# Kernel tuning notes

Measured on AMD Instinct MI355X. Metric: run time of the kernel, lower is better.

The kernel has to match this reference:

```python
import jax, jax.numpy as jnp
import numpy as np

B, L, D, E, K = 8, 384, 1024, 4, 2
H = 4 * D  # expert MLP hidden


def setup_inputs() -> dict:
    key = jax.random.key(0)
    ks = jax.random.split(key, 10)
    def w(k, shape, fan_in):
        return jax.random.normal(k, shape, jnp.float32) / np.sqrt(fan_in).astype(np.float32)
    return {
        "context_c": jax.random.normal(ks[0], (B, L, D), jnp.float32),
        "time_cond": jax.random.normal(ks[1], (B, D), jnp.float32),
        "gate_W": w(ks[2], (E, 3 * D), 3 * D),
        "gate_b": jnp.zeros((E,), jnp.float32),
        "tmod_W": w(ks[3], (2 * E, D), D),
        "tmod_b": jnp.zeros((2 * E,), jnp.float32),
        "eW1": w(ks[4], (E, D, H), D),
        "eb1": jnp.zeros((E, H), jnp.float32),
        "eW2": w(ks[5], (E, H, D), H),
        "eb2": jnp.zeros((E, D), jnp.float32),
        "sW1": w(ks[6], (D, H), D),
        "sb1": jnp.zeros((H,), jnp.float32),
        "sW2": w(ks[7], (H, D), H),
        "sb2": jnp.zeros((D,), jnp.float32),
    }


def reference(context_c, time_cond, gate_W, gate_b, tmod_W, tmod_b,
              eW1, eb1, eW2, eb2, sW1, sb1, sW2, sb2):
    Lh = Lw = L // 3
    Lp = L - Lh - Lw
    head = context_c[:, :Lh]            # (B, Lh, D)
    wrist = context_c[:, Lh:Lh + Lw]    # (B, Lw, D)
    prop = context_c[:, Lh + Lw:]       # (B, Lp, D)

    # per-sample modality-combo aggregates for the gate
    full_agg = context_c.mean(axis=1)
    hp_agg = (head.sum(axis=1) + prop.sum(axis=1)) / (Lh + Lp)
    wp_agg = (wrist.sum(axis=1) + prop.sum(axis=1)) / (Lw + Lp)
    gate_in = jnp.concatenate([full_agg, hp_agg, wp_agg], axis=-1)  # (B, 3D)

    logits = gate_in @ gate_W.T + gate_b                            # (B, E)
    mod = jax.nn.silu(time_cond) @ tmod_W.T + tmod_b                # (B, 2E)
    scale, shift = mod[:, :E], mod[:, E:]
    logits = logits * (1.0 + scale) + shift

    scores = jax.nn.softmax(logits, axis=-1)
    tw, ti = jax.lax.top_k(scores, K)                               # (B, K)
    tw = tw / (tw.sum(axis=-1, keepdims=True) + 1e-8)
    # per-sample combined weight for each expert: (B, E)
    w_be = (jax.nn.one_hot(ti, E, dtype=tw.dtype) * tw[..., None]).sum(axis=1)

    # modality mask per expert (E, L): expert 1 skips wrist, expert 2 skips head
    mask_np = np.ones((E, L), np.float32)
    mask_np[1, Lh:Lh + Lw] = 0.0
    mask_np[2, :Lh] = 0.0
    mask = jnp.asarray(mask_np)

    # run all experts on all tokens (token-wise MLP), combine with per-sample
    # routing weights and per-expert modality masks — identical math to the
    # original per-sample sliced dispatch.
    h = jax.nn.gelu(jnp.einsum('bld,edh->belh', context_c, eW1)
                    + eb1[None, :, None, :], approximate=True)      # (B,E,L,H)
    y = jnp.einsum('belh,ehd->beld', h, eW2) + eb2[None, :, None, :]
    out = jnp.einsum('be,el,beld->bld', w_be, mask, y)

    # shared expert (always-on)
    shared = jax.nn.gelu(context_c @ sW1 + sb1, approximate=True) @ sW2 + sb2
    return out + shared
```

## Files before the change

kernel.cpp:

```cpp
#include <hip/hip_runtime.h>
#include <cstdint>
#include <cstddef>


#define DEV __device__ __forceinline__

typedef __attribute__((ext_vector_type(8))) __bf16 bf16x8;
typedef __attribute__((ext_vector_type(4))) __bf16 bf16x4;
typedef __attribute__((ext_vector_type(4))) float f32x4;

static constexpr int Bb = 8, Ll = 384, Dd = 1024, Ee = 4, Hh = 4096;

DEV void load_lds16(const void* g, void* l) {
  __builtin_amdgcn_global_load_lds(
      (const __attribute__((address_space(1))) void*)g,
      (__attribute__((address_space(3))) void*)l, 16, 0, 0);
}

DEV float gelu_tanh(float x) {
  float u = 0.7978845608028654f * (x + 0.044715f * x * x * x);
  float t = 1.0f - 2.0f / (1.0f + __expf(2.0f * u));
  return 0.5f * x * (1.0f + t);
}

DEV float wave_red(float v) {
#pragma unroll
  for (int o = 32; o > 0; o >>= 1) v += __shfl_down(v, o, 64);
  return v;
}


__global__ void cvt_x_kernel(const float* __restrict__ src, __bf16* __restrict__ dst, int n4) {
  int i = blockIdx.x * blockDim.x + threadIdx.x;
  if (i >= n4) return;
  float4 v = ((const float4*)src)[i];
  bf16x4 o;
  o.x = (__bf16)v.x; o.y = (__bf16)v.y; o.z = (__bf16)v.z; o.w = (__bf16)v.w;
  ((bf16x4*)dst)[i] = o;
}

__global__ void transpose_cvt_kernel(const float* __restrict__ src, __bf16* __restrict__ dst,
                                     int nr, int nc) {
  __shared__ float t[32][33];
  size_t base = (size_t)blockIdx.z * nr * nc;
  src += base; dst += base;
  int x = threadIdx.x & 31, y = threadIdx.x >> 5;
  int c0 = blockIdx.x * 32, r0 = blockIdx.y * 32;
#pragma unroll
  for (int r = 0; r < 4; ++r) {
    int rr = y + r * 8;
    t[rr][x] = src[(size_t)(r0 + rr) * nc + c0 + x];
  }
  __syncthreads();
#pragma unroll
  for (int r = 0; r < 4; ++r) {
    int rr = y + r * 8;
    dst[(size_t)(c0 + rr) * nr + r0 + x] = (__bf16)t[x][rr];
  }
}


__global__ void agg_kernel(const float* __restrict__ ctx, float* __restrict__ part) {
  int c = blockIdx.x, b = blockIdx.y, t = threadIdx.x;
  int d0 = t * 4;
  float4 sum = {0.f, 0.f, 0.f, 0.f};
  const float* p = ctx + ((size_t)(b * Ll + c * 64)) * Dd + d0;
  for (int l = 0; l < 64; ++l) {
    float4 v = *(const float4*)(p + (size_t)l * Dd);
    sum.x += v.x; sum.y += v.y; sum.z += v.z; sum.w += v.w;
  }
  *(float4*)(part + ((size_t)(b * 6 + c)) * Dd + d0) = sum;
}

__global__ void gate_kernel(const float* __restrict__ part, const float* __restrict__ tc,
                            const float* __restrict__ gW, const float* __restrict__ gb,
                            const float* __restrict__ tW, const float* __restrict__ tb,
                            int* __restrict__ slotE, float* __restrict__ slotW) {
  __shared__ float gi[3 * Dd];
  __shared__ float st[Dd];
  __shared__ float red[12];
  int b = blockIdx.x, t = threadIdx.x;
  const float* pb = part + (size_t)b * 6 * Dd;
#pragma unroll
  for (int k = 0; k < 4; ++k) {
    int d = t * 4 + k;
    float p0 = pb[d], p1 = pb[Dd + d], p2 = pb[2 * Dd + d];
    float p3 = pb[3 * Dd + d], p4 = pb[4 * Dd + d], p5 = pb[5 * Dd + d];
    gi[d]          = (p0 + p1 + p2 + p3 + p4 + p5) * (1.0f / 384.0f);
    gi[Dd + d]     = (p0 + p1 + p4 + p5) * (1.0f / 256.0f);
    gi[2 * Dd + d] = (p2 + p3 + p4 + p5) * (1.0f / 256.0f);
    float tv = tc[b * Dd + d];
    st[d] = tv / (1.0f + __expf(-tv));
  }
  __syncthreads();
  int wid = t >> 6, lane = t & 63;
  float aL = 0.f;
  for (int i = lane; i < 3 * Dd; i += 64) aL += gi[i] * gW[wid * 3 * Dd + i];
  aL = wave_red(aL);
  float aA = 0.f, aB = 0.f;
  for (int i = lane; i < Dd; i += 64) {
    float s = st[i];
    aA += s * tW[wid * Dd + i];
    aB += s * tW[(wid + 4) * Dd + i];
  }
  aA = wave_red(aA); aB = wave_red(aB);
  if (lane == 0) { red[wid] = aL; red[4 + wid] = aA; red[8 + wid] = aB; }
  __syncthreads();
  if (t == 0) {
    float lg[4];
#pragma unroll
    for (int e = 0; e < 4; ++e) {
      float logit = red[e] + gb[e];
      float scale = red[4 + e] + tb[e];
      float shift = red[8 + e] + tb[4 + e];
      lg[e] = logit * (1.0f + scale) + shift;
    }
    float m = fmaxf(fmaxf(lg[0], lg[1]), fmaxf(lg[2], lg[3]));
    float p[4], sum = 0.f;
#pragma unroll
    for (int e = 0; e < 4; ++e) { p[e] = __expf(lg[e] - m); sum += p[e]; }
#pragma unroll
    for (int e = 0; e < 4; ++e) p[e] /= sum;
    int i0 = 0;
    for (int e = 1; e < 4; ++e) if (p[e] > p[i0]) i0 = e;
    int i1 = -1;
    for (int e = 0; e < 4; ++e) if (e != i0 && (i1 < 0 || p[e] > p[i1])) i1 = e;
    float sw = p[i0] + p[i1] + 1e-8f;
    slotE[b * 4 + 0] = i0; slotE[b * 4 + 1] = i1;
    slotW[b * 4 + 0] = p[i0] / sw; slotW[b * 4 + 1] = p[i1] / sw;
  }
}


__global__ __launch_bounds__(256) void gemm1_kernel(
    const __bf16* __restrict__ Xbf, const __bf16* __restrict__ W1T,
    const __bf16* __restrict__ S1T, const float* __restrict__ eb1,
    const float* __restrict__ sb1, const int* __restrict__ slotE,
    const float* __restrict__ slotW, __bf16* __restrict__ Hbuf, int bbase) {
  constexpr int K = Dd;
  int bid = blockIdx.x, nwg = gridDim.x;
  int lid = (bid & 7) * (nwg >> 3) + (bid >> 3);
  int nt = lid & 31;
  int r = lid >> 5;
  int mt = r % 3; r /= 3;
  int s = r % 3;
  int bl = r / 3;
  int b = bbase + bl;
  int e = (s == 2) ? Ee : slotE[b * 4 + s];
  if ((e == 1 && mt == 1) || (e == 2 && mt == 0)) return;
  float wgt = (s == 2) ? 1.0f : slotW[b * 4 + s];

  const __bf16* Ab = Xbf + ((size_t)(b * Ll + mt * 128)) * K;
  const __bf16* Bbp = (e < Ee ? W1T + (size_t)e * Hh * K : S1T) + (size_t)(nt * 128) * K;
  const float* b1p = (e < Ee ? eb1 + e * Hh : sb1);

  __shared__ __align__(16) char smem[65536];

  int tid = threadIdx.x, wid = tid >> 6, lane = tid & 63;
  int q = lane >> 4, l16 = lane & 15;
  int wm = wid >> 1, wn = wid & 1;

  const __bf16* gp[8];
  uint32_t lo[8];
#pragma unroll
  for (int u = 0; u < 8; ++u) {
    int c = wid * 8 + u;
    int isB = c >> 4;
    int blk = (c & 15) >> 1;
    int ks = c & 1;
    const __bf16* base = isB ? Bbp : Ab;
    gp[u] = base + (size_t)(blk * 16 + l16) * K + ks * 32 + q * 8;
    lo[u] = (uint32_t)(isB * 16384 + (blk * 2 + ks) * 1024);
  }

  f32x4 acc[4][4];
  f32x4 zero = {0.f, 0.f, 0.f, 0.f};
#pragma unroll
  for (int i = 0; i < 4; ++i)
#pragma unroll
    for (int j = 0; j < 4; ++j) acc[i][j] = zero;

#pragma unroll
  for (int u = 0; u < 8; ++u) load_lds16(gp[u], smem + lo[u]);

  constexpr int NK = K / 64;
  for (int kt = 0; kt < NK; ++kt) {
    int ph = kt & 1;
    __syncthreads();
    if (kt + 1 < NK) {
#pragma unroll
      for (int u = 0; u < 8; ++u) {
        gp[u] += 64;
        load_lds16(gp[u], smem + lo[u] + (ph ^ 1) * 32768);
      }
    }
    const char* sm = (const char*)smem + ph * 32768;
#pragma unroll
    for (int ks = 0; ks < 2; ++ks) {
      bf16x8 a[4], bb[4];
#pragma unroll
      for (int i = 0; i < 4; ++i)
        a[i] = *(const bf16x8*)(sm + (((wm * 4 + i) * 2 + ks) * 64 + lane) * 16);
#pragma unroll
      for (int j = 0; j < 4; ++j)
        bb[j] = *(const bf16x8*)(sm + 16384 + (((wn * 4 + j) * 2 + ks) * 64 + lane) * 16);
#pragma unroll
      for (int i = 0; i < 4; ++i)
#pragma unroll
        for (int j = 0; j < 4; ++j)
          acc[i][j] = __builtin_amdgcn_mfma_f32_16x16x32_bf16(a[i], bb[j], acc[i][j], 0, 0, 0);
    }
  }

  float bias[4];
#pragma unroll
  for (int j = 0; j < 4; ++j) bias[j] = b1p[nt * 128 + wn * 64 + j * 16 + l16];

  __syncthreads();
  __bf16* tile = (__bf16*)smem;
#pragma unroll
  for (int i = 0; i < 4; ++i)
#pragma unroll
    for (int j = 0; j < 4; ++j)
#pragma unroll
      for (int r2 = 0; r2 < 4; ++r2) {
        float x = acc[i][j][r2] + bias[j];
        int row = wm * 64 + i * 16 + q * 4 + r2;
        int col = wn * 64 + j * 16 + l16;
        tile[row * 136 + col] = (__bf16)(wgt * gelu_tanh(x));
      }
  __syncthreads();
  __bf16* Hrow = Hbuf + ((size_t)(bl * 3 + s) * Ll + mt * 128) * Hh + nt * 128;
#pragma unroll
  for (int t2 = 0; t2 < 8; ++t2) {
    int gidx = t2 * 256 + tid;
    int row = gidx >> 4, cg = gidx & 15;
    bf16x8 v = *(const bf16x8*)(tile + row * 136 + cg * 8);
    *(bf16x8*)(Hrow + (size_t)row * Hh + cg * 8) = v;
  }
}


template <int KC>
__global__ __launch_bounds__(256) void gemm2_kernel(
    const __bf16* __restrict__ Hbuf, const __bf16* __restrict__ W2T,
    const __bf16* __restrict__ S2T, const float* __restrict__ eb2,
    const float* __restrict__ sb2, const int* __restrict__ slotE,
    const float* __restrict__ slotW, float* __restrict__ out,
    __bf16* __restrict__ pbuf, int bbase, int bc) {
  constexpr int K = Hh;
  constexpr int NKC = Hh / KC;
  int bid = blockIdx.x, nwg = gridDim.x;
  int lid = (bid & 7) * (nwg >> 3) + (bid >> 3);
  int nt = lid & 7;
  int r = lid >> 3;
  int mt = r % 3; r /= 3;
  int kc = r % NKC;
  int bl = r / NKC;
  int b = bbase + bl;

  __shared__ __align__(16) char smem[65536];

  int tid = threadIdx.x, wid = tid >> 6, lane = tid & 63;
  int q = lane >> 4, l16 = lane & 15;
  int wm = wid >> 1, wn = wid & 1;

  f32x4 acc[4][4];
  f32x4 zero = {0.f, 0.f, 0.f, 0.f};
#pragma unroll
  for (int i = 0; i < 4; ++i)
#pragma unroll
    for (int j = 0; j < 4; ++j) acc[i][j] = zero;
  float biasacc[4] = {0.f, 0.f, 0.f, 0.f};

  for (int s = 0; s < 3; ++s) {
    int e = (s == 2) ? Ee : slotE[b * 4 + s];
    if ((e == 1 && mt == 1) || (e == 2 && mt == 0)) continue;
    float wgt = (s == 2) ? 1.0f : slotW[b * 4 + s];

    const __bf16* Ab = Hbuf + ((size_t)(bl * 3 + s) * Ll + mt * 128) * K + (size_t)kc * KC;
    const __bf16* Bbp = (e < Ee ? W2T + (size_t)e * Dd * K : S2T) + (size_t)(nt * 128) * K + (size_t)kc * KC;

    const __bf16* gp[8];
    uint32_t lo[8];
#pragma unroll
    for (int u = 0; u < 8; ++u) {
      int c = wid * 8 + u;
      int isB = c >> 4;
      int blk = (c & 15) >> 1;
      int ks = c & 1;
      const __bf16* base = isB ? Bbp : Ab;
      gp[u] = base + (size_t)(blk * 16 + l16) * K + ks * 32 + q * 8;
      lo[u] = (uint32_t)(isB * 16384 + (blk * 2 + ks) * 1024);
    }

#pragma unroll
    for (int u = 0; u < 8; ++u) load_lds16(gp[u], smem + lo[u]);

    constexpr int NK = KC / 64;
    for (int kt = 0; kt < NK; ++kt) {
      int ph = kt & 1;
      __syncthreads();
      if (kt + 1 < NK) {
#pragma unroll
        for (int u = 0; u < 8; ++u) {
          gp[u] += 64;
          load_lds16(gp[u], smem + lo[u] + (ph ^ 1) * 32768);
        }
      }
      const char* sm = (const char*)smem + ph * 32768;
#pragma unroll
      for (int ks = 0; ks < 2; ++ks) {
        bf16x8 a[4], bb[4];
#pragma unroll
        for (int i = 0; i < 4; ++i)
          a[i] = *(const bf16x8*)(sm + (((wm * 4 + i) * 2 + ks) * 64 + lane) * 16);
#pragma unroll
        for (int j = 0; j < 4; ++j)
          bb[j] = *(const bf16x8*)(sm + 16384 + (((wn * 4 + j) * 2 + ks) * 64 + lane) * 16);
#pragma unroll
        for (int i = 0; i < 4; ++i)
#pragma unroll
          for (int j = 0; j < 4; ++j)
            acc[i][j] = __builtin_amdgcn_mfma_f32_16x16x32_bf16(a[i], bb[j], acc[i][j], 0, 0, 0);
      }
    }

    if (kc == 0) {
      const float* b2p = (e < Ee ? eb2 + e * Dd : sb2);
#pragma unroll
      for (int j = 0; j < 4; ++j)
        biasacc[j] += wgt * b2p[nt * 128 + wn * 64 + j * 16 + l16];
    }
  }

  if (pbuf) {
    __syncthreads();
    __bf16* tile = (__bf16*)smem;
#pragma unroll
    for (int i = 0; i < 4; ++i)
#pragma unroll
      for (int j = 0; j < 4; ++j)
#pragma unroll
        for (int r2 = 0; r2 < 4; ++r2) {
          int row = wm * 64 + i * 16 + q * 4 + r2;
          int col = wn * 64 + j * 16 + l16;
          tile[row * 136 + col] = (__bf16)(acc[i][j][r2] + biasacc[j]);
        }
    __syncthreads();
    __bf16* Prow = pbuf + (((size_t)(kc * bc + bl) * Ll + mt * 128)) * Dd + nt * 128;
#pragma unroll
    for (int t2 = 0; t2 < 8; ++t2) {
      int gidx = t2 * 256 + tid;
      int row = gidx >> 4, cg = gidx & 15;
      bf16x8 v = *(const bf16x8*)(tile + row * 136 + cg * 8);
      *(bf16x8*)(Prow + (size_t)row * Dd + cg * 8) = v;
    }
  } else {
    float* orow = out + ((size_t)(b * Ll + mt * 128)) * Dd + nt * 128;
#pragma unroll
    for (int i = 0; i < 4; ++i)
#pragma unroll
      for (int j = 0; j < 4; ++j)
#pragma unroll
        for (int r2 = 0; r2 < 4; ++r2) {
          int row = wm * 64 + i * 16 + q * 4 + r2;
          int col = wn * 64 + j * 16 + l16;
          atomicAdd(orow + (size_t)row * Dd + col, acc[i][j][r2] + biasacc[j]);
        }
  }
}

__global__ void reduce_kernel(const __bf16* __restrict__ pbuf, float* __restrict__ out,
                              int n8, size_t stride, int nkc) {
  int i = blockIdx.x * blockDim.x + threadIdx.x;
  if (i >= n8) return;
  size_t base = (size_t)i * 8;
  float sum[8];
#pragma unroll
  for (int k = 0; k < 8; ++k) sum[k] = 0.f;
  for (int kc = 0; kc < nkc; ++kc) {
    bf16x8 v = *(const bf16x8*)(pbuf + kc * stride + base);
#pragma unroll
    for (int k = 0; k < 8; ++k) sum[k] += (float)v[k];
  }
  float4 o0 = {sum[0], sum[1], sum[2], sum[3]};
  float4 o1 = {sum[4], sum[5], sum[6], sum[7]};
  *(float4*)(out + base) = o0;
  *(float4*)(out + base + 4) = o1;
}


extern "C" void kernel_launch(void* const* d_in, const int* in_sizes, int n_in,
                              void* d_out, int out_size, void* d_ws, size_t ws_size,
                              hipStream_t stream) {
  (void)in_sizes; (void)n_in;
  const float* ctx = (const float*)d_in[0];
  const float* tc  = (const float*)d_in[1];
  const float* gW  = (const float*)d_in[2];
  const float* gb  = (const float*)d_in[3];
  const float* tW  = (const float*)d_in[4];
  const float* tb  = (const float*)d_in[5];
  const float* eW1 = (const float*)d_in[6];
  const float* eb1 = (const float*)d_in[7];
  const float* eW2 = (const float*)d_in[8];
  const float* eb2 = (const float*)d_in[9];
  const float* sW1 = (const float*)d_in[10];
  const float* sb1 = (const float*)d_in[11];
  const float* sW2 = (const float*)d_in[12];
  const float* sb2 = (const float*)d_in[13];
  float* out = (float*)d_out;

  char* ws = (char*)d_ws;
  size_t off = 0;
  auto alloc = [&](size_t sz) { size_t o = off; off += (sz + 255) & ~(size_t)255; return o; };
  size_t oW1T = alloc((size_t)Ee * Hh * Dd * 2);
  size_t oW2T = alloc((size_t)Ee * Dd * Hh * 2);
  size_t oS1T = alloc((size_t)Hh * Dd * 2);
  size_t oS2T = alloc((size_t)Dd * Hh * 2);
  size_t oX   = alloc((size_t)Bb * Ll * Dd * 2);
  size_t oP   = alloc((size_t)Bb * 6 * Dd * 4);
  size_t oSE  = alloc(Bb * 4 * sizeof(int));
  size_t oSW  = alloc(Bb * 4 * sizeof(float));
  size_t fixed = off;

  auto hbufB = [&](int bc) { return (size_t)bc * 3 * Ll * Hh * 2; };
  auto pbufB = [&](int bc, int nkc) { return (size_t)nkc * bc * Ll * Dd * 2; };
  int bc = 1; bool use_pbuf = false; int nkc = 4;
  if (fixed + hbufB(8) + pbufB(8, 8) + 512 <= ws_size)      { bc = 8; use_pbuf = true; nkc = 8; }
  else if (fixed + hbufB(8) + pbufB(8, 4) + 512 <= ws_size) { bc = 8; use_pbuf = true; nkc = 4; }
  else if (fixed + hbufB(4) + pbufB(4, 4) + 512 <= ws_size) { bc = 4; use_pbuf = true; nkc = 4; }
  else if (fixed + hbufB(4) + 512 <= ws_size)               { bc = 4; use_pbuf = false; nkc = 4; }
  else if (fixed + hbufB(2) + 512 <= ws_size)               { bc = 2; use_pbuf = false; nkc = 4; }
  else                                                      { bc = 1; use_pbuf = false; nkc = 4; }
  int nchunk = Bb / bc;
  size_t oH = alloc(hbufB(bc));
  size_t oPB = use_pbuf ? alloc(pbufB(bc, nkc)) : 0;

  __bf16* W1T = (__bf16*)(ws + oW1T);
  __bf16* W2T = (__bf16*)(ws + oW2T);
  __bf16* S1T = (__bf16*)(ws + oS1T);
  __bf16* S2T = (__bf16*)(ws + oS2T);
  __bf16* Xbf = (__bf16*)(ws + oX);
  float*  part = (float*)(ws + oP);
  int*    slotE = (int*)(ws + oSE);
  float*  slotW = (float*)(ws + oSW);
  __bf16* Hbuf = (__bf16*)(ws + oH);
  __bf16* Pbuf = use_pbuf ? (__bf16*)(ws + oPB) : nullptr;

  if (!use_pbuf)
    hipMemsetAsync(d_out, 0, (size_t)out_size * sizeof(float), stream);

  cvt_x_kernel<<<(Bb * Ll * Dd / 4 + 255) / 256, 256, 0, stream>>>(ctx, Xbf, Bb * Ll * Dd / 4);
  transpose_cvt_kernel<<<dim3(Hh / 32, Dd / 32, Ee), 256, 0, stream>>>(eW1, W1T, Dd, Hh);
  transpose_cvt_kernel<<<dim3(Dd / 32, Hh / 32, Ee), 256, 0, stream>>>(eW2, W2T, Hh, Dd);
  transpose_cvt_kernel<<<dim3(Hh / 32, Dd / 32, 1), 256, 0, stream>>>(sW1, S1T, Dd, Hh);
  transpose_cvt_kernel<<<dim3(Dd / 32, Hh / 32, 1), 256, 0, stream>>>(sW2, S2T, Hh, Dd);
  agg_kernel<<<dim3(6, Bb), 256, 0, stream>>>(ctx, part);
  gate_kernel<<<Bb, 256, 0, stream>>>(part, tc, gW, gb, tW, tb, slotE, slotW);

  for (int c = 0; c < nchunk; ++c) {
    gemm1_kernel<<<dim3(288 * bc), 256, 0, stream>>>(
        Xbf, W1T, S1T, eb1, sb1, slotE, slotW, Hbuf, c * bc);
    int g2 = 8 * 3 * nkc * bc;
    if (nkc == 8)
      gemm2_kernel<512><<<dim3(g2), 256, 0, stream>>>(
          Hbuf, W2T, S2T, eb2, sb2, slotE, slotW, out, Pbuf, c * bc, bc);
    else
      gemm2_kernel<1024><<<dim3(g2), 256, 0, stream>>>(
          Hbuf, W2T, S2T, eb2, sb2, slotE, slotW, out, Pbuf, c * bc, bc);
    if (use_pbuf) {
      int n8 = bc * Ll * Dd / 8;
      reduce_kernel<<<(n8 + 255) / 256, 256, 0, stream>>>(
          Pbuf, out + (size_t)c * bc * Ll * Dd, n8, (size_t)bc * Ll * Dd, nkc);
    }
  }
}
```

Baseline: 563.2 us.

## Drop LDS double buffering in expert GEMMs to raise occupancy

Both GEMM kernels switch from a double-buffered LDS pipeline (64 KB, prefetching the next K tile during compute) to a single 32 KB buffer (34816 bytes allocated) with load, sync, compute each step. Launch bounds now request 4 workgroups per CU. The aim is to hide global-load latency by running more resident waves instead of explicit prefetch. The cost is an extra barrier per K step and no intra-block overlap of loads with MFMA work.

Result: faster. 549.1 us (-2.5%).

```diff
diff --git a/kernel.cpp b/kernel.cpp
--- a/kernel.cpp
+++ b/kernel.cpp
@@ -132,7 +132,7 @@
 }
 
 
-__global__ __launch_bounds__(256) void gemm1_kernel(
+__global__ __launch_bounds__(256, 4) void gemm1_kernel(
     const __bf16* __restrict__ Xbf, const __bf16* __restrict__ W1T,
     const __bf16* __restrict__ S1T, const float* __restrict__ eb1,
     const float* __restrict__ sb1, const int* __restrict__ slotE,
@@ -154,7 +154,7 @@
   const __bf16* Bbp = (e < Ee ? W1T + (size_t)e * Hh * K : S1T) + (size_t)(nt * 128) * K;
   const float* b1p = (e < Ee ? eb1 + e * Hh : sb1);
 
-  __shared__ __align__(16) char smem[65536];
+  __shared__ __align__(16) char smem[34816];
 
   int tid = threadIdx.x, wid = tid >> 6, lane = tid & 63;
   int q = lane >> 4, l16 = lane & 15;
@@ -180,36 +180,28 @@
 #pragma unroll
     for (int j = 0; j < 4; ++j) acc[i][j] = zero;
 
-#pragma unroll
-  for (int u = 0; u < 8; ++u) load_lds16(gp[u], smem + lo[u]);
-
-  constexpr int NK = K / 64;
-  for (int kt = 0; kt < NK; ++kt) {
-    int ph = kt & 1;
+  for (int kt = 0; kt < K / 64; ++kt) {
     __syncthreads();
-    if (kt + 1 < NK) {
-#pragma unroll
-      for (int u = 0; u < 8; ++u) {
-        gp[u] += 64;
-        load_lds16(gp[u], smem + lo[u] + (ph ^ 1) * 32768);
-      }
-    }
-    const char* sm = (const char*)smem + ph * 32768;
+#pragma unroll
+    for (int u = 0; u < 8; ++u) load_lds16(gp[u], smem + lo[u]);
+    __syncthreads();
 #pragma unroll
     for (int ks = 0; ks < 2; ++ks) {
       bf16x8 a[4], bb[4];
 #pragma unroll
       for (int i = 0; i < 4; ++i)
-        a[i] = *(const bf16x8*)(sm + (((wm * 4 + i) * 2 + ks) * 64 + lane) * 16);
+        a[i] = *(const bf16x8*)(smem + (((wm * 4 + i) * 2 + ks) * 64 + lane) * 16);
 #pragma unroll
       for (int j = 0; j < 4; ++j)
-        bb[j] = *(const bf16x8*)(sm + 16384 + (((wn * 4 + j) * 2 + ks) * 64 + lane) * 16);
+        bb[j] = *(const bf16x8*)(smem + 16384 + (((wn * 4 + j) * 2 + ks) * 64 + lane) * 16);
 #pragma unroll
       for (int i = 0; i < 4; ++i)
 #pragma unroll
         for (int j = 0; j < 4; ++j)
           acc[i][j] = __builtin_amdgcn_mfma_f32_16x16x32_bf16(a[i], bb[j], acc[i][j], 0, 0, 0);
     }
+#pragma unroll
+    for (int u = 0; u < 8; ++u) gp[u] += 64;
   }
 
   float bias[4];
@@ -242,7 +234,7 @@
 
 
 template <int KC>
-__global__ __launch_bounds__(256) void gemm2_kernel(
+__global__ __launch_bounds__(256, 4) void gemm2_kernel(
     const __bf16* __restrict__ Hbuf, const __bf16* __restrict__ W2T,
     const __bf16* __restrict__ S2T, const float* __restrict__ eb2,
     const float* __restrict__ sb2, const int* __restrict__ slotE,
@@ -259,7 +251,7 @@
   int bl = r / NKC;
   int b = bbase + bl;
 
-  __shared__ __align__(16) char smem[65536];
+  __shared__ __align__(16) char smem[34816];
 
   int tid = threadIdx.x, wid = tid >> 6, lane = tid & 63;
   int q = lane >> 4, l16 = lane & 15;
@@ -294,36 +286,28 @@
       lo[u] = (uint32_t)(isB * 16384 + (blk * 2 + ks) * 1024);
     }
 
-#pragma unroll
-    for (int u = 0; u < 8; ++u) load_lds16(gp[u], smem + lo[u]);
-
-    constexpr int NK = KC / 64;
-    for (int kt = 0; kt < NK; ++kt) {
-      int ph = kt & 1;
+    for (int kt = 0; kt < KC / 64; ++kt) {
       __syncthreads();
-      if (kt + 1 < NK) {
-#pragma unroll
-        for (int u = 0; u < 8; ++u) {
-          gp[u] += 64;
-          load_lds16(gp[u], smem + lo[u] + (ph ^ 1) * 32768);
-        }
-      }
-      const char* sm = (const char*)smem + ph * 32768;
+#pragma unroll
+      for (int u = 0; u < 8; ++u) load_lds16(gp[u], smem + lo[u]);
+      __syncthreads();
 #pragma unroll
       for (int ks = 0; ks < 2; ++ks) {
         bf16x8 a[4], bb[4];
 #pragma unroll
         for (int i = 0; i < 4; ++i)
-          a[i] = *(const bf16x8*)(sm + (((wm * 4 + i) * 2 + ks) * 64 + lane) * 16);
+          a[i] = *(const bf16x8*)(smem + (((wm * 4 + i) * 2 + ks) * 64 + lane) * 16);
 #pragma unroll
         for (int j = 0; j < 4; ++j)
-          bb[j] = *(const bf16x8*)(sm + 16384 + (((wn * 4 + j) * 2 + ks) * 64 + lane) * 16);
+          bb[j] = *(const bf16x8*)(smem + 16384 + (((wn * 4 + j) * 2 + ks) * 64 + lane) * 16);
 #pragma unroll
         for (int i = 0; i < 4; ++i)
 #pragma unroll
           for (int j = 0; j < 4; ++j)
             acc[i][j] = __builtin_amdgcn_mfma_f32_16x16x32_bf16(a[i], bb[j], acc[i][j], 0, 0, 0);
       }
+#pragma unroll
+      for (int u = 0; u < 8; ++u) gp[u] += 64;
     }
 
     if (kc == 0) {
```
